# Kernel optimization log

Measured on AMD Instinct MI355X. Metric: run time of the kernel, lower is better.

## Reference

```python
import jax, jax.numpy as jnp
import numpy as np

NA = 4
NC = 60


def setup_inputs() -> dict:
    key = jax.random.key(0)
    k1, k2 = jax.random.split(key)
    bs, nG = 8, 128
    p = jax.random.normal(k1, (bs, NA * (5 + NC), nG, nG), dtype=jnp.float32)
    # anchor (w, h) in pixels; positive, realistic scale
    anchors = jax.random.uniform(k2, (NA, 2), dtype=jnp.float32) * 100.0 + 10.0
    return {"p": p, "anchors": anchors, "img_dim": 1024}


def reference(p, anchors, img_dim):
    bs = p.shape[0]
    nG = p.shape[2]
    nA = anchors.shape[0]
    nC = p.shape[1] // nA - 5
    stride = jnp.float32(img_dim) / nG

    # [bs, nA, nG, nG, 5+nC]
    p = p.reshape(bs, nA, 5 + nC, nG, nG).transpose(0, 1, 3, 4, 2)

    x = jax.nn.sigmoid(p[..., 0])
    y = jax.nn.sigmoid(p[..., 1])
    w = jax.nn.sigmoid(p[..., 2])
    h = jax.nn.sigmoid(p[..., 3])
    pred_conf = p[..., 4]
    pred_cls = p[..., 5:]

    grid = jnp.arange(nG, dtype=jnp.float32)
    grid_x = grid[None, None, None, :]   # broadcast over rows
    grid_y = grid[None, None, :, None]   # broadcast over cols
    scaled = anchors / stride            # [nA, 2]
    anchor_w = scaled[:, 0][None, :, None, None]
    anchor_h = scaled[:, 1][None, :, None, None]

    width = (w * 2.0) ** 2 * anchor_w
    height = (h * 2.0) ** 2 * anchor_h

    # [bs, nA, nG, nG, 4]
    pred_boxes = jnp.stack((x + grid_x, y + grid_y, width, height), axis=-1)

    output = jnp.concatenate(
        (
            pred_boxes.reshape(bs, -1, 4) * stride,
            jax.nn.sigmoid(pred_conf).reshape(bs, -1, 1),
            pred_cls.reshape(bs, -1, nC),
        ),
        axis=-1,
    )
    return output
```

## Files before the change

kernel.cpp:

```cpp
#include <hip/hip_runtime.h>


namespace {
constexpr int kNA  = 4;
constexpr int kNC  = 60;
constexpr int kNCH = kNC + 5;
constexpr int kNG  = 128;
constexpr int kTW  = 64;
constexpr int kThreads = 256;
constexpr int kRow = kNG * kNG;
}

__global__ __launch_bounds__(kThreads, 8)
void yolo_head_kernel(const float* __restrict__ p,
                      const float* __restrict__ anchors,
                      const int* __restrict__ img_dim,
                      float* __restrict__ out)
{
    __shared__ float tile[kTW * kNCH];

    const int blk  = blockIdx.x;
    const int half = blk & 1;
    const int gy   = (blk >> 1) & (kNG - 1);
    const int ba   = blk >> 8;
    const int a    = ba & (kNA - 1);
    const int b    = ba >> 2;
    const int gx0  = half * kTW;

    const float stride = (float)img_dim[0] / (float)kNG;
    const float aw4 = 4.0f * anchors[2 * a];
    const float ah4 = 4.0f * anchors[2 * a + 1];
    const float gyf = (float)gy;

    const int t = threadIdx.x;
    const float* __restrict__ pin =
        p + (((size_t)b * (kNA * kNCH) + (size_t)a * kNCH) * kNG + gy) * kNG + gx0;

    for (int l = t; l < kNCH * (kTW / 2); l += kThreads) {
        const int c    = l >> 5;
        const int col2 = l & 31;
        const int s    = col2 * 2;
        const float2 v = *reinterpret_cast<const float2*>(pin + (size_t)c * kRow + s);
        float r0 = v.x, r1 = v.y;
        if (c < 5) {
            const float s0 = 1.0f / (1.0f + expf(-v.x));
            const float s1 = 1.0f / (1.0f + expf(-v.y));
            if (c == 0) {
                r0 = (s0 + (float)(gx0 + s)) * stride;
                r1 = (s1 + (float)(gx0 + s + 1)) * stride;
            } else if (c == 1) {
                r0 = (s0 + gyf) * stride;
                r1 = (s1 + gyf) * stride;
            } else if (c == 2) {
                r0 = s0 * s0 * aw4;
                r1 = s1 * s1 * aw4;
            } else if (c == 3) {
                r0 = s0 * s0 * ah4;
                r1 = s1 * s1 * ah4;
            } else {
                r0 = s0;
                r1 = s1;
            }
        }
        tile[s * kNCH + c]       = r0;
        tile[(s + 1) * kNCH + c] = r1;
    }

    __syncthreads();

    float4* __restrict__ op = reinterpret_cast<float4*>(
        out + (size_t)((((b * kNA + a) * kNG + gy) * kNG) + gx0) * kNCH);
    const float4* tp = reinterpret_cast<const float4*>(tile);
    for (int l = t; l < (kTW * kNCH) / 4; l += kThreads)
        op[l] = tp[l];
}

extern "C" void kernel_launch(void* const* d_in, const int* in_sizes, int n_in,
                              void* d_out, int out_size, void* d_ws, size_t ws_size,
                              hipStream_t stream)
{
    const float* p       = (const float*)d_in[0];
    const float* anchors = (const float*)d_in[1];
    const int*   img_dim = (const int*)d_in[2];
    float* out = (float*)d_out;

    const int bs = in_sizes[0] / (kNA * kNCH * kNG * kNG);
    const int nblocks = bs * kNA * kNG * 2;
    yolo_head_kernel<<<nblocks, kThreads, 0, stream>>>(p, anchors, img_dim, out);
}
```

Measured before the change: 241.0 us.

## Process full grid rows per block with float4 loads batched into registers

Each block now transposes a full 128-column row for one anchor instead of half a row, using 512 threads. Global reads are widened from float2 to float4 and all loads are issued up front into a register array before any compute or shared-memory writes, to expose more memory-level parallelism. The shared tile doubles to about 33KB and the block count halves, which may reduce occupancy. Scattered shared-memory writes with stride 65 may also change bank-conflict behaviour.

```diff
diff --git a/kernel.cpp b/kernel.cpp
--- a/kernel.cpp
+++ b/kernel.cpp
@@ -6,9 +6,10 @@
 constexpr int kNC  = 60;
 constexpr int kNCH = kNC + 5;
 constexpr int kNG  = 128;
-constexpr int kTW  = 64;
-constexpr int kThreads = 256;
-constexpr int kRow = kNG * kNG;
+constexpr int kThreads = 512;
+constexpr int kRow  = kNG * kNG;
+constexpr int kItems = kNCH * (kNG / 4);
+constexpr int kIter  = (kItems + kThreads - 1) / kThreads;
 }
 
 __global__ __launch_bounds__(kThreads, 8)
@@ -17,15 +18,13 @@
                       const int* __restrict__ img_dim,
                       float* __restrict__ out)
 {
-    __shared__ float tile[kTW * kNCH];
+    __shared__ float tile[kNG * kNCH];
 
-    const int blk  = blockIdx.x;
-    const int half = blk & 1;
-    const int gy   = (blk >> 1) & (kNG - 1);
-    const int ba   = blk >> 8;
-    const int a    = ba & (kNA - 1);
-    const int b    = ba >> 2;
-    const int gx0  = half * kTW;
+    const int blk = blockIdx.x;
+    const int gy  = blk & (kNG - 1);
+    const int ba  = blk >> 7;
+    const int a   = ba & (kNA - 1);
+    const int b   = ba >> 2;
 
     const float stride = (float)img_dim[0] / (float)kNG;
     const float aw4 = 4.0f * anchors[2 * a];
@@ -34,45 +33,50 @@
 
     const int t = threadIdx.x;
     const float* __restrict__ pin =
-        p + (((size_t)b * (kNA * kNCH) + (size_t)a * kNCH) * kNG + gy) * kNG + gx0;
+        p + (((size_t)b * (kNA * kNCH) + (size_t)a * kNCH) * kNG + gy) * kNG;
 
-    for (int l = t; l < kNCH * (kTW / 2); l += kThreads) {
-        const int c    = l >> 5;
-        const int col2 = l & 31;
-        const int s    = col2 * 2;
-        const float2 v = *reinterpret_cast<const float2*>(pin + (size_t)c * kRow + s);
-        float r0 = v.x, r1 = v.y;
+    float4 v[kIter];
+    #pragma unroll
+    for (int i = 0; i < kIter; ++i) {
+        const int l = t + i * kThreads;
+        if (l < kItems)
+            v[i] = *reinterpret_cast<const float4*>(
+                pin + (size_t)(l >> 5) * kRow + (size_t)(l & 31) * 4);
+    }
+
+    #pragma unroll
+    for (int i = 0; i < kIter; ++i) {
+        const int l = t + i * kThreads;
+        if (l >= kItems) continue;
+        const int c = l >> 5;
+        const int s = (l & 31) * 4;
+        float r[4] = {v[i].x, v[i].y, v[i].z, v[i].w};
         if (c < 5) {
-            const float s0 = 1.0f / (1.0f + expf(-v.x));
-            const float s1 = 1.0f / (1.0f + expf(-v.y));
-            if (c == 0) {
-                r0 = (s0 + (float)(gx0 + s)) * stride;
-                r1 = (s1 + (float)(gx0 + s + 1)) * stride;
-            } else if (c == 1) {
-                r0 = (s0 + gyf) * stride;
-                r1 = (s1 + gyf) * stride;
-            } else if (c == 2) {
-                r0 = s0 * s0 * aw4;
-                r1 = s1 * s1 * aw4;
-            } else if (c == 3) {
-                r0 = s0 * s0 * ah4;
-                r1 = s1 * s1 * ah4;
-            } else {
-                r0 = s0;
-                r1 = s1;
+            #pragma unroll
+            for (int j = 0; j < 4; ++j) {
+                const float sg = 1.0f / (1.0f + expf(-r[j]));
+                if (c == 0)      r[j] = (sg + (float)(s + j)) * stride;
+                else if (c == 1) r[j] = (sg + gyf) * stride;
+                else if (c == 2) r[j] = sg * sg * aw4;
+                else if (c == 3) r[j] = sg * sg * ah4;
+                else             r[j] = sg;
             }
         }
-        tile[s * kNCH + c]       = r0;
-        tile[(s + 1) * kNCH + c] = r1;
+        #pragma unroll
+        for (int j = 0; j < 4; ++j)
+            tile[(s + j) * kNCH + c] = r[j];
     }
 
     __syncthreads();
 
     float4* __restrict__ op = reinterpret_cast<float4*>(
-        out + (size_t)((((b * kNA + a) * kNG + gy) * kNG) + gx0) * kNCH);
+        out + (size_t)(((b * kNA + a) * kNG + gy) * kNG) * kNCH);
     const float4* tp = reinterpret_cast<const float4*>(tile);
-    for (int l = t; l < (kTW * kNCH) / 4; l += kThreads)
-        op[l] = tp[l];
+    #pragma unroll
+    for (int i = 0; i < kIter; ++i) {
+        const int l = t + i * kThreads;
+        if (l < kItems) op[l] = tp[l];
+    }
 }
 
 extern "C" void kernel_launch(void* const* d_in, const int* in_sizes, int n_in,
@@ -85,6 +89,6 @@
     float* out = (float*)d_out;
 
     const int bs = in_sizes[0] / (kNA * kNCH * kNG * kNG);
-    const int nblocks = bs * kNA * kNG * 2;
+    const int nblocks = bs * kNA * kNG;
     yolo_head_kernel<<<nblocks, kThreads, 0, stream>>>(p, anchors, img_dim, out);
 }
```

New measurement: 237.2 us. Within noise of the previous version (-1.6%).
